# Kernel tuning notes

Hardware: AMD Instinct MI355X
Metric: run time of the kernel (lower is better)

Reference implementation:

```python
import jax, jax.numpy as jnp
import numpy as np

P = 16
D = 768          # latent_dim
H = 3072         # hidden_dim
B = 256
OUT_DIMS = [100 + 10 * i for i in range(P)]   # sum = 2800
MAX_OUT = max(OUT_DIMS)
EPS = 1e-5


def setup_inputs() -> dict:
    key = jax.random.key(0)
    ks = jax.random.split(key, 6)
    x = jax.random.normal(ks[0], (B, P, D), dtype=jnp.float32)
    # LayerNorm params per part (torch default init: gamma=1, beta=0)
    gamma = jnp.ones((P, D), dtype=jnp.float32)
    beta = jnp.zeros((P, D), dtype=jnp.float32)
    # fc1: Linear(D, H, bias=False) per part -> stacked [P, H, D]
    w1 = jax.random.normal(ks[1], (P, H, D), dtype=jnp.float32) * 0.02
    # fc2: Linear(H, out_dims[i], bias=True) per part, padded to MAX_OUT.
    # Padded rows are never read (sliced away at concat).
    w2 = jax.random.normal(ks[2], (P, MAX_OUT, H), dtype=jnp.float32) * 0.02
    b2 = jnp.zeros((P, MAX_OUT), dtype=jnp.float32)
    return {"x": x, "gamma": gamma, "beta": beta, "w1": w1, "w2": w2, "b2": b2}


def reference(x, gamma, beta, w1, w2, b2):
    # Per-part LayerNorm over latent dim (torch uses biased variance)
    mu = jnp.mean(x, axis=-1, keepdims=True)
    var = jnp.mean(jnp.square(x - mu), axis=-1, keepdims=True)
    xn = (x - mu) * jax.lax.rsqrt(var + EPS) * gamma[None] + beta[None]  # [B,P,D]
    # fc1 (no bias) + exact GELU (torch.nn.GELU default)
    h = jnp.einsum('bpd,phd->bph', xn, w1)          # [B,P,H]
    h = jax.nn.gelu(h, approximate=False)
    # dropout p=0.0 -> identity
    # fc2 (with bias), padded grouped GEMM
    out_full = jnp.einsum('bph,poh->bpo', h, w2) + b2[None]  # [B,P,MAX_OUT]
    # concat variable-width slices along last dim
    out = jnp.concatenate([out_full[:, i, :OUT_DIMS[i]] for i in range(P)], axis=-1)
    return out  # [B, sum(OUT_DIMS)] = [256, 2800]
```

## Files before the change

kernel.cpp:

```cpp
#include <hip/hip_runtime.h>
#include <math.h>

typedef unsigned short u16;
typedef unsigned int u32;
typedef __attribute__((ext_vector_type(4))) float f32x4;
typedef __attribute__((ext_vector_type(8))) short bf16x8;

#define NP 16
#define DLAT 768
#define HDIM 3072
#define NB 256
#define MAXO 250
#define TOT 2800

__device__ __forceinline__ u16 f2b(float f) {
  union { float f; u32 u; } v; v.f = f;
  u32 u = v.u;
  u32 r = (u + 0x7fffu + ((u >> 16) & 1u)) >> 16;
  return (u16)r;
}

__device__ __forceinline__ u32 cvtpk(float lo, float hi) {
  u32 r;
  asm("v_cvt_pk_bf16_f32 %0, %1, %2" : "=v"(r) : "v"(lo), "v"(hi));
  return r;
}

__device__ __forceinline__ void gll16(const void* g, void* l) {
  __builtin_amdgcn_global_load_lds(
      (const __attribute__((address_space(1))) void*)g,
      (__attribute__((address_space(3))) void*)l, 16, 0, 0);
}

__global__ __launch_bounds__(256) void ln_kernel(
    const float* __restrict__ x, const float* __restrict__ gamma,
    const float* __restrict__ beta, u16* __restrict__ xn) {
  const int wave = threadIdx.x >> 6, lane = threadIdx.x & 63;
  const int row = blockIdx.x * 4 + wave;
  const int b = row >> 4, p = row & 15;
  const float4* xr = (const float4*)(x + (size_t)row * DLAT);
  const float4* g4 = (const float4*)(gamma + (size_t)p * DLAT);
  const float4* b4 = (const float4*)(beta + (size_t)p * DLAT);
  float4 v[3];
  float s = 0.f, ss = 0.f;
#pragma unroll
  for (int j = 0; j < 3; ++j) {
    v[j] = xr[lane + j * 64];
    s += v[j].x + v[j].y + v[j].z + v[j].w;
    ss += v[j].x * v[j].x + v[j].y * v[j].y + v[j].z * v[j].z + v[j].w * v[j].w;
  }
#pragma unroll
  for (int o = 32; o; o >>= 1) { s += __shfl_xor(s, o); ss += __shfl_xor(ss, o); }
  const float mu = s * (1.f / 768.f);
  const float var = ss * (1.f / 768.f) - mu * mu;
  const float rstd = rsqrtf(var + 1e-5f);
  u16* xo = xn + ((size_t)(p * NB + b)) * DLAT;
#pragma unroll
  for (int j = 0; j < 3; ++j) {
    const int f = lane + j * 64;
    float4 g = g4[f], be = b4[f];
    float o0 = (v[j].x - mu) * rstd * g.x + be.x;
    float o1 = (v[j].y - mu) * rstd * g.y + be.y;
    float o2 = (v[j].z - mu) * rstd * g.z + be.z;
    float o3 = (v[j].w - mu) * rstd * g.w + be.w;
    uint2 w;
    w.x = (u32)f2b(o0) | ((u32)f2b(o1) << 16);
    w.y = (u32)f2b(o2) | ((u32)f2b(o3) << 16);
    *(uint2*)&xo[f * 4] = w;
  }
}

__global__ __launch_bounds__(256) void fc1_kernel(
    const u16* __restrict__ xn, const float* __restrict__ w1, u16* __restrict__ h) {
  const int bid = blockIdx.x;
  const int xcd = bid & 7;
  const int j = bid >> 3;
  const int p = xcd * 2 + (j >= 48 ? 1 : 0);
  const int jj = j % 48;
  const int n0 = (jj >> 1) * 128;
  const int m0 = (jj & 1) * 128;

  const int tid = threadIdx.x;
  const int lane = tid & 63, wave = tid >> 6;
  const int lanelo = lane & 15, lanehi = lane >> 4;
  const int wr = wave >> 1, wc = wave & 1;

  const u16* Ap = xn + (size_t)p * NB * DLAT + (size_t)m0 * DLAT;
  const float* Bp = w1 + (size_t)p * HDIM * DLAT + (size_t)n0 * DLAT;

  __shared__ u16 As[128 * 64];
  __shared__ float Bs[128 * 64];

  int a_src[4], b_src[8];
#pragma unroll
  for (int jx = 0; jx < 4; ++jx) {
    const int s = tid + 256 * jx, r = s >> 3, c = s & 7;
    a_src[jx] = r * DLAT + ((c ^ (r & 7)) << 3);
  }
#pragma unroll
  for (int jx = 0; jx < 8; ++jx) {
    const int s = tid + 256 * jx, r = s >> 4, c = s & 15;
    b_src[jx] = r * DLAT + ((c ^ (r & 7)) << 2);
  }

  f32x4 acc[4][4] = {};
  const int st = bid % 12;

  for (int cc = 0; cc < 12; ++cc) {
    const int ch = (cc + st) % 12;
    const int k2 = ch * 64;
#pragma unroll
    for (int jx = 0; jx < 4; ++jx)
      gll16(Ap + a_src[jx] + k2, &As[(tid + 256 * jx) * 8]);
#pragma unroll
    for (int jx = 0; jx < 8; ++jx)
      gll16(Bp + b_src[jx] + k2, &Bs[(tid + 256 * jx) * 4]);
    __syncthreads();
#pragma unroll
    for (int kt = 0; kt < 2; ++kt) {
      bf16x8 af[4], bf[4];
#pragma unroll
      for (int m = 0; m < 4; ++m) {
        const int ra = wr * 64 + m * 16 + lanelo;
        af[m] = *(const bf16x8*)&As[ra * 64 + (((kt * 4 + lanehi) ^ (ra & 7)) << 3)];
      }
#pragma unroll
      for (int n = 0; n < 4; ++n) {
        const int rb = wc * 64 + n * 16 + lanelo;
        const int c0 = kt * 8 + lanehi * 2;
        const float4 f0 = *(const float4*)&Bs[rb * 64 + ((c0 ^ (rb & 7)) << 2)];
        const float4 f1 = *(const float4*)&Bs[rb * 64 + (((c0 + 1) ^ (rb & 7)) << 2)];
        union { u32 u[4]; bf16x8 v; } t;
        t.u[0] = cvtpk(f0.x, f0.y); t.u[1] = cvtpk(f0.z, f0.w);
        t.u[2] = cvtpk(f1.x, f1.y); t.u[3] = cvtpk(f1.z, f1.w);
        bf[n] = t.v;
      }
#pragma unroll
      for (int m = 0; m < 4; ++m)
#pragma unroll
        for (int n = 0; n < 4; ++n)
          acc[m][n] = __builtin_amdgcn_mfma_f32_16x16x32_bf16(af[m], bf[n], acc[m][n], 0, 0, 0);
    }
    __syncthreads();
  }

  u16* hp = h + (size_t)p * NB * HDIM;
#pragma unroll
  for (int m = 0; m < 4; ++m) {
#pragma unroll
    for (int n = 0; n < 4; ++n) {
      const int col = n0 + wc * 64 + n * 16 + lanelo;
#pragma unroll
      for (int r = 0; r < 4; ++r) {
        const int row = m0 + wr * 64 + m * 16 + lanehi * 4 + r;
        const float vv = acc[m][n][r];
        const float gel = 0.5f * vv * (1.f + erff(vv * 0.70710678118654752f));
        hp[(size_t)row * HDIM + col] = f2b(gel);
      }
    }
  }
}

__global__ __launch_bounds__(256) void fc2_kernel(
    const u16* __restrict__ hbuf, const float* __restrict__ w2,
    const float* __restrict__ b2, float* __restrict__ out) {
  const int bid = blockIdx.x;
  const int bs = (bid & 7) * 32 + (bid >> 3);
  const int p = bs >> 4;
  const int mb = (bs >> 2) & 3;
  const int nb = bs & 3;
  const int odim = 100 + 10 * p;
  const int n0 = nb * 64;
  if (n0 >= odim) return;
  const int m0 = mb * 64;
  const int off = 100 * p + 5 * p * (p - 1);

  const int tid = threadIdx.x;
  const int lane = tid & 63, wave = tid >> 6;
  const int lanelo = lane & 15, lanehi = lane >> 4;
  const int wr = wave >> 1, wc = wave & 1;

  const u16* Ap = hbuf + (size_t)p * NB * HDIM + (size_t)m0 * HDIM;
  const float* Bp = w2 + (size_t)p * MAXO * HDIM;

  __shared__ u16 As[3][64 * 32];
  __shared__ u16 Bs[2][64 * 32];

  int ag_off;
  const int ag_base = (64 * wave) * 8;
  {
    int slot = 64 * wave + lane;
    int r = slot >> 2;
    int c = (slot & 3) ^ ((r >> 1) & 3);
    ag_off = r * HDIM + c * 8;
  }
  const int br0 = min(n0 + (tid >> 3), MAXO - 1);
  const int br1 = min(n0 + (tid >> 3) + 32, MAXO - 1);
  const float* bg0 = Bp + (size_t)br0 * HDIM + (tid & 7) * 4;
  const float* bg1 = Bp + (size_t)br1 * HDIM + (tid & 7) * 4;
  int bso[2];
#pragma unroll
  for (int i = 0; i < 2; ++i) {
    int r = (tid >> 3) + 32 * i;
    int c = ((tid & 7) >> 1) ^ ((r >> 1) & 3);
    bso[i] = (r * 4 + c) * 8 + (tid & 1) * 4;
  }
  int a_sl[2], b_sl[2];
#pragma unroll
  for (int m = 0; m < 2; ++m) {
    int r = wr * 32 + m * 16 + lanelo;
    a_sl[m] = (r * 4 + (lanehi ^ ((r >> 1) & 3))) * 8;
    int rb = wc * 32 + m * 16 + lanelo;
    b_sl[m] = (rb * 4 + (lanehi ^ ((rb >> 1) & 3))) * 8;
  }

  f32x4 acc[2][2] = {};
  float4 bA0, bA1, bB0, bB1;
  const int NK = HDIM / 32;

  auto issue = [&](int kt, float4& r0, float4& r1) {
    const int k2 = kt * 32;
    gll16(Ap + ag_off + k2, &As[kt % 3][ag_base]);
    asm volatile("" ::: "memory");
    r0 = *(const float4*)(bg0 + k2);
    r1 = *(const float4*)(bg1 + k2);
    asm volatile("" ::: "memory");
  };

  auto step = [&](int kt, float4& r0, float4& r1) {
    if (kt + 1 < NK) asm volatile("s_waitcnt vmcnt(3)" ::: "memory");
    else             asm volatile("s_waitcnt vmcnt(0)" ::: "memory");
    {
      u16* bb = &Bs[kt & 1][0];
      uint2 w0, w1v;
      w0.x = (u32)f2b(r0.x) | ((u32)f2b(r0.y) << 16);
      w0.y = (u32)f2b(r0.z) | ((u32)f2b(r0.w) << 16);
      w1v.x = (u32)f2b(r1.x) | ((u32)f2b(r1.y) << 16);
      w1v.y = (u32)f2b(r1.z) | ((u32)f2b(r1.w) << 16);
      *(uint2*)&bb[bso[0]] = w0;
      *(uint2*)&bb[bso[1]] = w1v;
    }
    asm volatile("s_waitcnt lgkmcnt(0)" ::: "memory");
    __builtin_amdgcn_s_barrier();
    asm volatile("" ::: "memory");
    if (kt + 2 < NK) issue(kt + 2, r0, r1);
    const u16* a_ = &As[kt % 3][0];
    const u16* b_ = &Bs[kt & 1][0];
    bf16x8 af[2], bf[2];
#pragma unroll
    for (int m = 0; m < 2; ++m) af[m] = *(const bf16x8*)&a_[a_sl[m]];
#pragma unroll
    for (int n = 0; n < 2; ++n) bf[n] = *(const bf16x8*)&b_[b_sl[n]];
#pragma unroll
    for (int m = 0; m < 2; ++m)
#pragma unroll
      for (int n = 0; n < 2; ++n)
        acc[m][n] = __builtin_amdgcn_mfma_f32_16x16x32_bf16(af[m], bf[n], acc[m][n], 0, 0, 0);
  };

  issue(0, bA0, bA1);
  issue(1, bB0, bB1);
  for (int kt = 0; kt < NK; kt += 2) {
    step(kt, bA0, bA1);
    step(kt + 1, bB0, bB1);
  }

#pragma unroll
  for (int m = 0; m < 2; ++m) {
#pragma unroll
    for (int n = 0; n < 2; ++n) {
      const int col = n0 + wc * 32 + n * 16 + lanelo;
      if (col < odim) {
        const float bias = b2[(size_t)p * MAXO + col];
#pragma unroll
        for (int r = 0; r < 4; ++r) {
          const int row = m0 + wr * 32 + m * 16 + lanehi * 4 + r;
          out[(size_t)row * TOT + off + col] = acc[m][n][r] + bias;
        }
      }
    }
  }
}

extern "C" void kernel_launch(void* const* d_in, const int* in_sizes, int n_in,
                              void* d_out, int out_size, void* d_ws, size_t ws_size,
                              hipStream_t stream) {
  const float* x = (const float*)d_in[0];
  const float* gamma = (const float*)d_in[1];
  const float* beta = (const float*)d_in[2];
  const float* w1 = (const float*)d_in[3];
  const float* w2 = (const float*)d_in[4];
  const float* b2 = (const float*)d_in[5];
  float* out = (float*)d_out;

  u16* xn = (u16*)d_ws;
  u16* h = (u16*)d_ws + (size_t)NP * NB * DLAT;

  ln_kernel<<<1024, 256, 0, stream>>>(x, gamma, beta, xn);
  fc1_kernel<<<768, 256, 0, stream>>>(xn, w1, h);
  fc2_kernel<<<NP * 16, 256, 0, stream>>>(h, w2, b2, out);
}
```

Baseline: 119.1 us.

## Double-buffer fc1 LDS tiles with K=32 chunks to overlap loads and MFMA

Splits the fc1 K loop into 24 chunks of 32 and stages them through two LDS buffers, prefetching chunk ch+2 while computing chunk ch. Manual vmcnt waits and raw barriers replace __syncthreads so global loads stay in flight across compute. It also drops the per-block rotated K start and changes the A swizzle for the narrower rows. In exchange there are twice as many barriers per K and more sensitivity to the hand-counted vmcnt values.

```diff
diff --git a/kernel.cpp b/kernel.cpp
--- a/kernel.cpp
+++ b/kernel.cpp
@@ -88,48 +88,53 @@
   const u16* Ap = xn + (size_t)p * NB * DLAT + (size_t)m0 * DLAT;
   const float* Bp = w1 + (size_t)p * HDIM * DLAT + (size_t)n0 * DLAT;
 
-  __shared__ u16 As[128 * 64];
-  __shared__ float Bs[128 * 64];
-
-  int a_src[4], b_src[8];
+  __shared__ u16 As[2][128 * 32];
+  __shared__ float Bs[2][128 * 32];
+
+  int a_src[2], b_src[4];
+#pragma unroll
+  for (int jx = 0; jx < 2; ++jx) {
+    const int s = tid + 256 * jx, r = s >> 2, c = s & 3;
+    a_src[jx] = r * DLAT + ((c ^ ((r >> 1) & 3)) << 3);
+  }
 #pragma unroll
   for (int jx = 0; jx < 4; ++jx) {
     const int s = tid + 256 * jx, r = s >> 3, c = s & 7;
-    a_src[jx] = r * DLAT + ((c ^ (r & 7)) << 3);
-  }
-#pragma unroll
-  for (int jx = 0; jx < 8; ++jx) {
-    const int s = tid + 256 * jx, r = s >> 4, c = s & 15;
     b_src[jx] = r * DLAT + ((c ^ (r & 7)) << 2);
   }
 
+  auto stage = [&](int ch, int buf) {
+    const int k2 = ch * 32;
+#pragma unroll
+    for (int jx = 0; jx < 2; ++jx)
+      gll16(Ap + a_src[jx] + k2, &As[buf][(tid + 256 * jx) * 8]);
+#pragma unroll
+    for (int jx = 0; jx < 4; ++jx)
+      gll16(Bp + b_src[jx] + k2, &Bs[buf][(tid + 256 * jx) * 4]);
+  };
+
   f32x4 acc[4][4] = {};
-  const int st = bid % 12;
-
-  for (int cc = 0; cc < 12; ++cc) {
-    const int ch = (cc + st) % 12;
-    const int k2 = ch * 64;
-#pragma unroll
-    for (int jx = 0; jx < 4; ++jx)
-      gll16(Ap + a_src[jx] + k2, &As[(tid + 256 * jx) * 8]);
-#pragma unroll
-    for (int jx = 0; jx < 8; ++jx)
-      gll16(Bp + b_src[jx] + k2, &Bs[(tid + 256 * jx) * 4]);
-    __syncthreads();
-#pragma unroll
-    for (int kt = 0; kt < 2; ++kt) {
+  stage(0, 0);
+  stage(1, 1);
+
+  for (int ch = 0; ch < 24; ++ch) {
+    if (ch < 23) asm volatile("s_waitcnt vmcnt(6)" ::: "memory");
+    else         asm volatile("s_waitcnt vmcnt(0)" ::: "memory");
+    __builtin_amdgcn_s_barrier();
+    asm volatile("" ::: "memory");
+    const int cur = ch & 1;
+    {
       bf16x8 af[4], bf[4];
 #pragma unroll
       for (int m = 0; m < 4; ++m) {
         const int ra = wr * 64 + m * 16 + lanelo;
-        af[m] = *(const bf16x8*)&As[ra * 64 + (((kt * 4 + lanehi) ^ (ra & 7)) << 3)];
+        af[m] = *(const bf16x8*)&As[cur][ra * 32 + ((lanehi ^ ((ra >> 1) & 3)) << 3)];
       }
 #pragma unroll
       for (int n = 0; n < 4; ++n) {
         const int rb = wc * 64 + n * 16 + lanelo;
-        const int c0 = kt * 8 + lanehi * 2;
-        const float4 f0 = *(const float4*)&Bs[rb * 64 + ((c0 ^ (rb & 7)) << 2)];
-        const float4 f1 = *(const float4*)&Bs[rb * 64 + (((c0 + 1) ^ (rb & 7)) << 2)];
+        const float4 f0 = *(const float4*)&Bs[cur][rb * 32 + (((lanehi * 2 + 0) ^ (rb & 7)) << 2)];
+        const float4 f1 = *(const float4*)&Bs[cur][rb * 32 + (((lanehi * 2 + 1) ^ (rb & 7)) << 2)];
         union { u32 u[4]; bf16x8 v; } t;
         t.u[0] = cvtpk(f0.x, f0.y); t.u[1] = cvtpk(f0.z, f0.w);
         t.u[2] = cvtpk(f1.x, f1.y); t.u[3] = cvtpk(f1.z, f1.w);
@@ -141,7 +146,10 @@
         for (int n = 0; n < 4; ++n)
           acc[m][n] = __builtin_amdgcn_mfma_f32_16x16x32_bf16(af[m], bf[n], acc[m][n], 0, 0, 0);
     }
-    __syncthreads();
+    asm volatile("" ::: "memory");
+    __builtin_amdgcn_s_barrier();
+    asm volatile("" ::: "memory");
+    if (ch + 2 < 24) stage(ch + 2, cur);
   }
 
   u16* hp = h + (size_t)p * NB * HDIM;
```

Result: faster. 104.8 us (-12.0%).
